# Kernel optimization log

Hardware: AMD Instinct MI355X
Metric: run time of the kernel (lower is better)

Reference implementation:

```python
import jax, jax.numpy as jnp
import numpy as np

B, T, C = 1, 4096, 2048
NH, HS, NQG = 16, 128, 4          # n_head, head_size, n_query_groups (GQA)
Q_PER_KV = NH // NQG              # 4
QKV_DIM = (NH + 2 * NQG) * HS     # 3072
ROT = HS // 2                     # rotary half-dim = 64


def setup_inputs() -> dict:
    key = jax.random.key(0)
    k0, k1, k2 = jax.random.split(key, 3)
    x = jax.random.normal(k0, (B, T, C), dtype=jnp.float32)
    W_attn = jax.random.normal(k1, (QKV_DIM, C), dtype=jnp.float32) * 0.02
    W_proj = jax.random.normal(k2, (C, C), dtype=jnp.float32) * 0.02
    # RoPE cache: cos/sin of shape (T, head_size/2), flash-attn convention
    inv_freq = 1.0 / (10000.0 ** (jnp.arange(0, HS, 2, dtype=jnp.float32) / HS))
    freqs = jnp.arange(T, dtype=jnp.float32)[:, None] * inv_freq[None, :]
    return {"x": x, "cos": jnp.cos(freqs), "sin": jnp.sin(freqs),
            "W_attn": W_attn, "W_proj": W_proj}


def _apply_rope(t, cos, sin):
    # t: (B, T, H, HS); cos/sin: (T, ROT). Non-interleaved (rotate-half) form.
    x1, x2 = t[..., :ROT], t[..., ROT:]
    c = cos[None, :, None, :]
    s = sin[None, :, None, :]
    return jnp.concatenate([x1 * c - x2 * s, x2 * c + x1 * s], axis=-1)


def reference(x, cos, sin, W_attn, W_proj):
    Bx, Tx, Cx = x.shape
    qkv = jnp.einsum('btc,fc->btf', x, W_attn)                 # (B,T,3072)
    qkv = qkv.reshape(Bx, Tx, NQG, Q_PER_KV + 2, HS)
    q = qkv[:, :, :, :Q_PER_KV, :].reshape(Bx, Tx, NH, HS)     # (B,T,16,128)
    k = qkv[:, :, :, Q_PER_KV, :]                              # (B,T,4,128)
    v = qkv[:, :, :, Q_PER_KV + 1, :]                          # (B,T,4,128)
    q = _apply_rope(q, cos, sin)
    k = _apply_rope(k, cos, sin)
    # GQA: expand kv groups to match query heads (repeat_interleave on head dim)
    k = jnp.repeat(k, Q_PER_KV, axis=2)                        # (B,T,16,128)
    v = jnp.repeat(v, Q_PER_KV, axis=2)
    scale = 1.0 / np.sqrt(HS).astype(np.float32)
    scores = jnp.einsum('bthd,bshd->bhts', q, k) * scale       # (B,H,T,T)
    causal = jnp.tril(jnp.ones((Tx, Tx), dtype=bool))
    scores = jnp.where(causal[None, None], scores, jnp.finfo(scores.dtype).min)
    attn = jax.nn.softmax(scores, axis=-1)
    y = jnp.einsum('bhts,bshd->bthd', attn, v).reshape(Bx, Tx, Cx)
    return jnp.einsum('btc,oc->bto', y, W_proj)
```

## Files before the change

kernel.cpp:

```cpp
#include <hip/hip_runtime.h>
#include <hip/hip_bf16.h>

typedef __hip_bfloat16 bf16;
typedef __attribute__((ext_vector_type(8))) short short8;
typedef __attribute__((ext_vector_type(4))) short short4v;
typedef __attribute__((ext_vector_type(4))) float floatx4;

#define T_SEQ 4096
#define C_DIM 2048
#define NHEAD 16
#define HSZ   128
#define NGRP  4

#define MFMA_BF16(A,B,C) __builtin_amdgcn_mfma_f32_16x16x32_bf16((A),(B),(C),0,0,0)

__device__ __forceinline__ void gld_lds16(const bf16* g, bf16* l) {
  __builtin_amdgcn_global_load_lds(
      (__attribute__((address_space(1))) void*)(g),
      (__attribute__((address_space(3))) void*)(l), 16, 0, 0);
}

__global__ void cvt_kernel(const float* __restrict__ src, bf16* __restrict__ dst, long n)
{
  const long i = ((long)blockIdx.x * blockDim.x + threadIdx.x) * 8;
  if (i >= n) return;
  const float4 a = *(const float4*)(src + i);
  const float4 b = *(const float4*)(src + i + 4);
  bf16 tmp[8];
  tmp[0] = __float2bfloat16(a.x); tmp[1] = __float2bfloat16(a.y);
  tmp[2] = __float2bfloat16(a.z); tmp[3] = __float2bfloat16(a.w);
  tmp[4] = __float2bfloat16(b.x); tmp[5] = __float2bfloat16(b.y);
  tmp[6] = __float2bfloat16(b.z); tmp[7] = __float2bfloat16(b.w);
  *(short8*)(dst + i) = *(const short8*)tmp;
}

__global__ __launch_bounds__(256, 3)
void gemm_bt_kernel(const bf16* __restrict__ A, const bf16* __restrict__ B,
                    float* __restrict__ Cf, bf16* __restrict__ Cq,
                    bf16* __restrict__ Ck, bf16* __restrict__ Cvt,
                    int K, int qkv_mode)
{
  __shared__ alignas(16) bf16 As[128 * 64];
  __shared__ alignas(16) bf16 Bs[128 * 64];

  const int t  = threadIdx.x;
  const int w  = t >> 6, l = t & 63;
  const int wr = w >> 1, wc = w & 1;
  const int q4 = l >> 4, ln = l & 15;
  const long bm = (long)blockIdx.y * 128;
  const long bn = (long)blockIdx.x * 128;

  floatx4 acc[4][4] = {};

  const bf16* Ab = A + (bm + t / 8) * (long)K + (t % 8) * 8;
  const bf16* Bb = B + (bn + t / 8) * (long)K + (t % 8) * 8;

  for (int k0 = 0; k0 < K; k0 += 64) {
    __syncthreads();
#pragma unroll
    for (int i = 0; i < 4; ++i) {
      gld_lds16(Ab + (long)i * 32 * K + k0, As + (i * 256 + w * 64) * 8);
      gld_lds16(Bb + (long)i * 32 * K + k0, Bs + (i * 256 + w * 64) * 8);
    }
    __syncthreads();
#pragma unroll
    for (int kk = 0; kk < 64; kk += 32) {
      short8 af[4], bfr[4];
      const int co = kk + q4 * 8;
#pragma unroll
      for (int mi = 0; mi < 4; ++mi)
        af[mi] = *(const short8*)(As + (wr * 64 + mi * 16 + ln) * 64 + co);
#pragma unroll
      for (int ni = 0; ni < 4; ++ni)
        bfr[ni] = *(const short8*)(Bs + (wc * 64 + ni * 16 + ln) * 64 + co);
#pragma unroll
      for (int mi = 0; mi < 4; ++mi)
#pragma unroll
        for (int ni = 0; ni < 4; ++ni)
          acc[mi][ni] = MFMA_BF16(af[mi], bfr[ni], acc[mi][ni]);
    }
  }

  if (!qkv_mode) {
#pragma unroll
    for (int mi = 0; mi < 4; ++mi) {
      const long r0 = bm + wr * 64 + mi * 16 + q4 * 4;
#pragma unroll
      for (int ni = 0; ni < 4; ++ni) {
        const long c = bn + wc * 64 + ni * 16 + ln;
#pragma unroll
        for (int r = 0; r < 4; ++r)
          Cf[(r0 + r) * C_DIM + c] = acc[mi][ni][r];
      }
    }
  } else {
    const int cb = blockIdx.x;
    const int g = cb / 6, slot = cb - g * 6;
    if (slot == 5) {
      bf16* dstv = Cvt + (long)g * HSZ * T_SEQ;
#pragma unroll
      for (int pass = 0; pass < 2; ++pass) {
        __syncthreads();
        if (wc == pass) {
#pragma unroll
          for (int mi = 0; mi < 4; ++mi) {
            const int tc = wr * 64 + mi * 16 + q4 * 4;
#pragma unroll
            for (int ni = 0; ni < 4; ++ni) {
              const int dr = ni * 16 + ln;
              short4v pk;
#pragma unroll
              for (int r = 0; r < 4; ++r) {
                bf16 v = __float2bfloat16(acc[mi][ni][r]);
                pk[r] = *(short*)&v;
              }
              *(short4v*)(As + dr * 128 + tc) = pk;
            }
          }
        }
        __syncthreads();
        const int row = t >> 2, ch = (t & 3) * 32;
        bf16* gp = dstv + (long)(pass * 64 + row) * T_SEQ + bm + ch;
#pragma unroll
        for (int jj = 0; jj < 4; ++jj)
          *(short8*)(gp + jj * 8) = *(const short8*)(As + row * 128 + ch + jj * 8);
      }
    } else {
      bf16* dst = (slot < 4) ? (Cq + (long)(g * 4 + slot) * T_SEQ * HSZ)
                             : (Ck + (long)g * T_SEQ * HSZ);
#pragma unroll
      for (int mi = 0; mi < 4; ++mi) {
        const long r0 = bm + wr * 64 + mi * 16 + q4 * 4;
#pragma unroll
        for (int ni = 0; ni < 4; ++ni) {
          const long c = wc * 64 + ni * 16 + ln;
#pragma unroll
          for (int r = 0; r < 4; ++r)
            dst[(r0 + r) * HSZ + c] = __float2bfloat16(acc[mi][ni][r]);
        }
      }
    }
  }
}

__global__ void rope_kernel(bf16* __restrict__ Q, bf16* __restrict__ Kb,
                            const float* __restrict__ cs, const float* __restrict__ sn)
{
  const long idx = (long)blockIdx.x * blockDim.x + threadIdx.x;
  const long NQ = (long)NHEAD * T_SEQ * 8;
  bf16* buf; long rem; float qs;
  if (idx < NQ) { buf = Q;  rem = idx;      qs = 0.08838834764831845f * 1.4426950408889634f; }
  else          { buf = Kb; rem = idx - NQ; qs = 1.0f; }
  const int d0 = (int)(rem & 7) * 8;
  const int tt = (int)((rem >> 3) & (T_SEQ - 1));
  const int hh = (int)(rem >> 15);
  const float4 c0 = *(const float4*)(cs + tt * 64 + d0);
  const float4 c1 = *(const float4*)(cs + tt * 64 + d0 + 4);
  const float4 s0 = *(const float4*)(sn + tt * 64 + d0);
  const float4 s1 = *(const float4*)(sn + tt * 64 + d0 + 4);
  float cc[8] = {c0.x,c0.y,c0.z,c0.w,c1.x,c1.y,c1.z,c1.w};
  float ss[8] = {s0.x,s0.y,s0.z,s0.w,s1.x,s1.y,s1.z,s1.w};
  bf16* p = buf + ((long)hh * T_SEQ + tt) * HSZ + d0;
  short8 v1 = *(const short8*)(p);
  short8 v2 = *(const short8*)(p + 64);
  short8 o1, o2;
#pragma unroll
  for (int jj = 0; jj < 8; ++jj) {
    short u1 = v1[jj], u2 = v2[jj];
    const float x1 = __bfloat162float(*(bf16*)&u1);
    const float x2 = __bfloat162float(*(bf16*)&u2);
    bf16 y1 = __float2bfloat16((x1 * cc[jj] - x2 * ss[jj]) * qs);
    bf16 y2 = __float2bfloat16((x2 * cc[jj] + x1 * ss[jj]) * qs);
    o1[jj] = *(short*)&y1; o2[jj] = *(short*)&y2;
  }
  *(short8*)(p)      = o1;
  *(short8*)(p + 64) = o2;
}

__global__ __launch_bounds__(256, 2)
void attn_kernel(const bf16* __restrict__ Qg, const bf16* __restrict__ Kg,
                 const bf16* __restrict__ Vtg, bf16* __restrict__ Y,
                 bf16* __restrict__ Opart, float* __restrict__ Lpart)
{
  __shared__ alignas(16) bf16 Ks[64][132];
  __shared__ alignas(16) bf16 Vt[128][68];
  __shared__ alignas(16) bf16 Ps[128][68];

  const int id  = blockIdx.x;
  const int h   = id >> 5;
  const int r   = id & 31;
  const int c   = r >> 1;
  const int isA = r & 1;
  const int g   = h >> 2;

  const int t = threadIdx.x;
  const int w = t >> 6, l = t & 63;
  const int q4 = l >> 4, ln = l & 15;

  const bf16* Qh = Qg + (long)h * T_SEQ * HSZ;
  const bf16* Kh = Kg + (long)g * T_SEQ * HSZ;
  const bf16* Vh = Vtg + (long)g * HSZ * T_SEQ;

  short8 ones_f;
#pragma unroll
  for (int i = 0; i < 8; ++i) ones_f[i] = (ln == 0) ? (short)0x3F80 : (short)0;

  const int krow = t >> 4, kc = (t & 15) * 8;
  const int vrow = t >> 3, vc = (t & 7) * 8;

  const int nph = isA ? 2 : 1;
  for (int ph = 0; ph < nph; ++ph) {
    const int P      = (isA && ph == 0) ? c : (31 - c);
    const int jlo    = (isA && ph == 1) ? 33 : 0;
    const int jhi    = isA ? (ph == 0 ? (2 * c + 2) : (64 - 2 * c)) : 33;
    const bool direct = (isA && ph == 0);
    const int qbase  = P * 128 + w * 32;

    short8 qf[2][4];
#pragma unroll
    for (int mi = 0; mi < 2; ++mi) {
      const long row = qbase + mi * 16 + ln;
#pragma unroll
      for (int ks = 0; ks < 4; ++ks)
        qf[mi][ks] = *(const short8*)(Qh + row * HSZ + ks * 32 + q4 * 8);
    }

    floatx4 acc[2][8] = {};
    floatx4 acc_l[2] = {};

    short8 kpre[4], vpre[4];
    {
      const int sb = jlo * 64;
#pragma unroll
      for (int i = 0; i < 4; ++i) {
        kpre[i] = *(const short8*)(Kh + (long)(sb + krow + 16 * i) * HSZ + kc);
        vpre[i] = *(const short8*)(Vh + (long)(vrow + 32 * i) * T_SEQ + sb + vc);
      }
    }

    for (int j = jlo; j < jhi; ++j) {
      const int s0 = j * 64;
#pragma unroll
      for (int i = 0; i < 4; ++i) {
        *(short8*)(&Ks[krow + 16 * i][kc]) = kpre[i];
        *(short8*)(&Vt[vrow + 32 * i][vc]) = vpre[i];
      }
      __syncthreads();
      if (j + 1 < jhi) {
        const int s1 = s0 + 64;
#pragma unroll
        for (int i = 0; i < 4; ++i) {
          kpre[i] = *(const short8*)(Kh + (long)(s1 + krow + 16 * i) * HSZ + kc);
          vpre[i] = *(const short8*)(Vh + (long)(vrow + 32 * i) * T_SEQ + s1 + vc);
        }
      }

      floatx4 sacc[2][4] = {};
#pragma unroll
      for (int ks = 0; ks < 4; ++ks) {
        short8 kf[4];
#pragma unroll
        for (int ni = 0; ni < 4; ++ni)
          kf[ni] = *(const short8*)(&Ks[ni * 16 + ln][ks * 32 + q4 * 8]);
#pragma unroll
        for (int mi = 0; mi < 2; ++mi)
#pragma unroll
          for (int ni = 0; ni < 4; ++ni)
            sacc[mi][ni] = MFMA_BF16(qf[mi][ks], kf[ni], sacc[mi][ni]);
      }

#pragma unroll
      for (int mi = 0; mi < 2; ++mi) {
        const int base_m = qbase + mi * 16 + q4 * 4 - s0 - ln;
#pragma unroll
        for (int ni = 0; ni < 4; ++ni)
#pragma unroll
          for (int r2 = 0; r2 < 4; ++r2) {
            float pv = __builtin_amdgcn_exp2f(sacc[mi][ni][r2]);
            if (base_m + r2 - ni * 16 < 0) pv = 0.f;
            Ps[w * 32 + mi * 16 + q4 * 4 + r2][ni * 16 + ln] = __float2bfloat16(pv);
          }
      }

#pragma unroll
      for (int ks = 0; ks < 2; ++ks) {
        short8 pf[2], vf[8];
#pragma unroll
        for (int mi = 0; mi < 2; ++mi)
          pf[mi] = *(const short8*)(&Ps[w * 32 + mi * 16 + ln][ks * 32 + q4 * 8]);
#pragma unroll
        for (int nd = 0; nd < 8; ++nd)
          vf[nd] = *(const short8*)(&Vt[nd * 16 + ln][ks * 32 + q4 * 8]);
#pragma unroll
        for (int mi = 0; mi < 2; ++mi) {
          acc_l[mi] = MFMA_BF16(pf[mi], ones_f, acc_l[mi]);
#pragma unroll
          for (int nd = 0; nd < 8; ++nd)
            acc[mi][nd] = MFMA_BF16(pf[mi], vf[nd], acc[mi][nd]);
        }
      }
      __syncthreads();
    }

    if (direct) {
#pragma unroll
      for (int mi = 0; mi < 2; ++mi) {
#pragma unroll
        for (int r2 = 0; r2 < 4; ++r2) {
          const float lv = __shfl(acc_l[mi][r2], l & 48, 64);
          const float inv = (lv > 0.f) ? 1.f / lv : 0.f;
          const long tq = qbase + mi * 16 + q4 * 4 + r2;
#pragma unroll
          for (int nd = 0; nd < 8; ++nd)
            Y[tq * C_DIM + h * HSZ + nd * 16 + ln] = __float2bfloat16(acc[mi][nd][r2] * inv);
        }
      }
    } else {
      const int sidx = (h * 16 + (15 - c)) * 2 + isA;
      bf16* Op = Opart + (long)sidx * (128 * 128);
      float* Lp = Lpart + sidx * 128;
#pragma unroll
      for (int mi = 0; mi < 2; ++mi) {
#pragma unroll
        for (int r2 = 0; r2 < 4; ++r2) {
          const int row = w * 32 + mi * 16 + q4 * 4 + r2;
          if (ln == 0) Lp[row] = acc_l[mi][r2];
#pragma unroll
          for (int nd = 0; nd < 8; ++nd)
            Op[row * 128 + nd * 16 + ln] = __float2bfloat16(acc[mi][nd][r2]);
        }
      }
    }
  }
}

__global__ void combine_kernel(const bf16* __restrict__ Opart,
                               const float* __restrict__ Lpart,
                               bf16* __restrict__ Y)
{
  const int b = blockIdx.x;
  const int h = b >> 4, pp = b & 15;
  const bf16* O0 = Opart + (long)b * 2 * 16384;
  const bf16* O1 = O0 + 16384;
  const float* L0 = Lpart + b * 256;
  const float* L1 = L0 + 128;
  const long qb = (long)(pp + 16) * 128;
  const int t = threadIdx.x;
#pragma unroll
  for (int it = 0; it < 8; ++it) {
    const int idx = it * 2048 + t * 8;
    const int row = idx >> 7, d = idx & 127;
    const float lsum = L0[row] + L1[row];
    const float inv = (lsum > 0.f) ? 1.f / lsum : 0.f;
    const short8 a = *(const short8*)(O0 + idx);
    const short8 bb = *(const short8*)(O1 + idx);
    short8 o;
#pragma unroll
    for (int jj = 0; jj < 8; ++jj) {
      short ua = a[jj], ub = bb[jj];
      const float fa = __bfloat162float(*(bf16*)&ua);
      const float fb = __bfloat162float(*(bf16*)&ub);
      bf16 y = __float2bfloat16((fa + fb) * inv);
      o[jj] = *(short*)&y;
    }
    *(short8*)(Y + (qb + row) * C_DIM + h * HSZ + d) = o;
  }
}

extern "C" void kernel_launch(void* const* d_in, const int* in_sizes, int n_in,
                              void* d_out, int out_size, void* d_ws, size_t ws_size,
                              hipStream_t stream)
{
  const float* x  = (const float*)d_in[0];
  const float* cs = (const float*)d_in[1];
  const float* sn = (const float*)d_in[2];
  const float* Wa = (const float*)d_in[3];
  const float* Wp = (const float*)d_in[4];
  float* out = (float*)d_out;

  const long nx  = (long)T_SEQ * C_DIM;
  const long nwa = (long)(NHEAD + 2 * NGRP) * HSZ * C_DIM;
  const long nwp = (long)C_DIM * C_DIM;
  const long nqh = (long)NHEAD * T_SEQ * HSZ;
  const long nkg = (long)NGRP * T_SEQ * HSZ;

  const size_t need = (size_t)(nx + nwa + nqh + 2 * nkg + nqh) * sizeof(bf16);
  if (ws_size < need) return;

  bf16* xb  = (bf16*)d_ws;
  bf16* Wab = xb + nx;
  bf16* Q   = Wab + nwa;
  bf16* K   = Q + nqh;
  bf16* Vt  = K + nkg;
  bf16* Y   = Vt + nkg;
  bf16* Wpb = Q;
  bf16* Opart = xb;
  float* Lpart = (float*)Wab;

  cvt_kernel<<<(int)(nx  / 8 / 256), 256, 0, stream>>>(x,  xb,  nx);
  cvt_kernel<<<(int)(nwa / 8 / 256), 256, 0, stream>>>(Wa, Wab, nwa);
  gemm_bt_kernel<<<dim3(24, 32), 256, 0, stream>>>(xb, Wab, nullptr, Q, K, Vt, C_DIM, 1);
  rope_kernel<<<2560, 256, 0, stream>>>(Q, K, cs, sn);
  attn_kernel<<<512, 256, 0, stream>>>(Q, K, Vt, Y, Opart, Lpart);
  combine_kernel<<<256, 256, 0, stream>>>(Opart, Lpart, Y);
  cvt_kernel<<<(int)(nwp / 8 / 256), 256, 0, stream>>>(Wp, Wpb, nwp);
  gemm_bt_kernel<<<dim3(16, 32), 256, 0, stream>>>(Y, Wpb, out, nullptr, nullptr, nullptr, C_DIM, 0);
}
```

Measured before the change: 335.6 us.

## Split causal attention work into three balanced slices per query-block pair

Replaces the two-way split of each causal query-block pair with a three-way split of KV ranges, so 768 attention blocks each get about 22 KV tiles. The combine kernel is generalized to sum 2 or 3 partial outputs per query block. Launch bounds are raised to 3 blocks per CU to fit the larger grid in one wave on the 256-CU device. The aim is better load balance and occupancy, at the cost of more partial-output traffic and register pressure.

```diff
diff --git a/kernel.cpp b/kernel.cpp
--- a/kernel.cpp
+++ b/kernel.cpp
@@ -177,7 +177,7 @@
   *(short8*)(p + 64) = o2;
 }
 
-__global__ __launch_bounds__(256, 2)
+__global__ __launch_bounds__(256, 3)
 void attn_kernel(const bf16* __restrict__ Qg, const bf16* __restrict__ Kg,
                  const bf16* __restrict__ Vtg, bf16* __restrict__ Y,
                  bf16* __restrict__ Opart, float* __restrict__ Lpart)
@@ -187,11 +187,34 @@
   __shared__ alignas(16) bf16 Ps[128][68];
 
   const int id  = blockIdx.x;
-  const int h   = id >> 5;
-  const int r   = id & 31;
-  const int c   = r >> 1;
-  const int isA = r & 1;
+  const int h   = id / 48;
+  const int r   = id - h * 48;
+  const int c   = r / 3;
+  const int sl  = r - c * 3;
   const int g   = h >> 2;
+
+  int segP[2], segLo[2], segHi[2], segPs[2], nseg;
+  bool segDir[2] = {false, false};
+  if (c <= 10) {
+    if (sl == 0) { nseg = 2;
+      segP[0] = c;      segLo[0] = 0;  segHi[0] = 2 * c + 2; segPs[0] = 0; segDir[0] = true;
+      segP[1] = 31 - c; segLo[1] = 44; segHi[1] = 64 - 2 * c; segPs[1] = 0;
+    } else if (sl == 1) { nseg = 1;
+      segP[0] = 31 - c; segLo[0] = 0;  segHi[0] = 22; segPs[0] = 1;
+    } else { nseg = 1;
+      segP[0] = 31 - c; segLo[0] = 22; segHi[0] = 44; segPs[0] = 2;
+    }
+  } else {
+    if (sl == 0) { nseg = 1;
+      segP[0] = c;      segLo[0] = 0;  segHi[0] = 22; segPs[0] = 0;
+    } else if (sl == 1) { nseg = 2;
+      segP[0] = c;      segLo[0] = 22; segHi[0] = 2 * c + 2;  segPs[0] = 1;
+      segP[1] = 31 - c; segLo[1] = 0;  segHi[1] = 42 - 2 * c; segPs[1] = 2;
+    } else { nseg = 1;
+      segP[0] = 31 - c; segLo[0] = 42 - 2 * c; segHi[0] = 64 - 2 * c; segPs[0] = 3;
+    }
+  }
+  const int pairBase = h * 53 + ((c <= 10) ? c * 3 : 33 + (c - 11) * 4);
 
   const int t = threadIdx.x;
   const int w = t >> 6, l = t & 63;
@@ -208,13 +231,11 @@
   const int krow = t >> 4, kc = (t & 15) * 8;
   const int vrow = t >> 3, vc = (t & 7) * 8;
 
-  const int nph = isA ? 2 : 1;
-  for (int ph = 0; ph < nph; ++ph) {
-    const int P      = (isA && ph == 0) ? c : (31 - c);
-    const int jlo    = (isA && ph == 1) ? 33 : 0;
-    const int jhi    = isA ? (ph == 0 ? (2 * c + 2) : (64 - 2 * c)) : 33;
-    const bool direct = (isA && ph == 0);
-    const int qbase  = P * 128 + w * 32;
+  for (int ph = 0; ph < nseg; ++ph) {
+    const int P   = segP[ph];
+    const int jlo = segLo[ph], jhi = segHi[ph];
+    const bool direct = segDir[ph];
+    const int qbase = P * 128 + w * 32;
 
     short8 qf[2][4];
 #pragma unroll
@@ -316,7 +337,7 @@
         }
       }
     } else {
-      const int sidx = (h * 16 + (15 - c)) * 2 + isA;
+      const int sidx = pairBase + segPs[ph];
       bf16* Op = Opart + (long)sidx * (128 * 128);
       float* Lp = Lpart + sidx * 128;
 #pragma unroll
@@ -338,29 +359,40 @@
                                const float* __restrict__ Lpart,
                                bf16* __restrict__ Y)
 {
-  const int b = blockIdx.x;
-  const int h = b >> 4, pp = b & 15;
-  const bf16* O0 = Opart + (long)b * 2 * 16384;
-  const bf16* O1 = O0 + 16384;
-  const float* L0 = Lpart + b * 256;
-  const float* L1 = L0 + 128;
-  const long qb = (long)(pp + 16) * 128;
+  const int cid = blockIdx.x;
+  const int h = cid / 21, u = cid - h * 21;
+  int P, sbase, ns;
+  if (u < 11) {
+    const int c = u; P = 31 - c; sbase = h * 53 + c * 3; ns = 3;
+  } else {
+    const int v = u - 11;
+    const int c = 11 + (v >> 1);
+    const int pb = h * 53 + 33 + (c - 11) * 4;
+    if (!(v & 1)) { P = c;      sbase = pb;     ns = 2; }
+    else          { P = 31 - c; sbase = pb + 2; ns = 2; }
+  }
+  const long qb = (long)P * 128;
   const int t = threadIdx.x;
 #pragma unroll
   for (int it = 0; it < 8; ++it) {
     const int idx = it * 2048 + t * 8;
     const int row = idx >> 7, d = idx & 127;
-    const float lsum = L0[row] + L1[row];
+    float lsum = 0.f;
+    float osum[8] = {0.f, 0.f, 0.f, 0.f, 0.f, 0.f, 0.f, 0.f};
+    for (int k = 0; k < ns; ++k) {
+      lsum += Lpart[(sbase + k) * 128 + row];
+      const short8 a = *(const short8*)(Opart + (long)(sbase + k) * 16384 + idx);
+#pragma unroll
+      for (int jj = 0; jj < 8; ++jj) {
+        short ua = a[jj];
+        osum[jj] += __bfloat162float(*(bf16*)&ua);
+      }
+    }
     const float inv = (lsum > 0.f) ? 1.f / lsum : 0.f;
-    const short8 a = *(const short8*)(O0 + idx);
-    const short8 bb = *(const short8*)(O1 + idx);
     short8 o;
 #pragma unroll
     for (int jj = 0; jj < 8; ++jj) {
-      short ua = a[jj], ub = bb[jj];
-      const float fa = __bfloat162float(*(bf16*)&ua);
-      const float fb = __bfloat162float(*(bf16*)&ub);
-      bf16 y = __float2bfloat16((fa + fb) * inv);
+      bf16 y = __float2bfloat16(osum[jj] * inv);
       o[jj] = *(short*)&y;
     }
     *(short8*)(Y + (qb + row) * C_DIM + h * HSZ + d) = o;
@@ -395,14 +427,14 @@
   bf16* Y   = Vt + nkg;
   bf16* Wpb = Q;
   bf16* Opart = xb;
-  float* Lpart = (float*)Wab;
+  float* Lpart = (float*)(xb + 848L * 16384);
 
   cvt_kernel<<<(int)(nx  / 8 / 256), 256, 0, stream>>>(x,  xb,  nx);
   cvt_kernel<<<(int)(nwa / 8 / 256), 256, 0, stream>>>(Wa, Wab, nwa);
   gemm_bt_kernel<<<dim3(24, 32), 256, 0, stream>>>(xb, Wab, nullptr, Q, K, Vt, C_DIM, 1);
   rope_kernel<<<2560, 256, 0, stream>>>(Q, K, cs, sn);
-  attn_kernel<<<512, 256, 0, stream>>>(Q, K, Vt, Y, Opart, Lpart);
-  combine_kernel<<<256, 256, 0, stream>>>(Opart, Lpart, Y);
+  attn_kernel<<<768, 256, 0, stream>>>(Q, K, Vt, Y, Opart, Lpart);
+  combine_kernel<<<336, 256, 0, stream>>>(Opart, Lpart, Y);
   cvt_kernel<<<(int)(nwp / 8 / 256), 256, 0, stream>>>(Wp, Wpb, nwp);
   gemm_bt_kernel<<<dim3(16, 32), 256, 0, stream>>>(Y, Wpb, out, nullptr, nullptr, nullptr, C_DIM, 0);
 }
```

Result: slower. 463.2 us (+38.0%).

## Fuse RoPE and Q scaling into the QKV GEMM epilogue

Applied to the files above, without the earlier changes.

Removes the standalone RoPE kernel and applies the rotary embedding and query scaling inside the QKV GEMM epilogue. The accumulator tile is staged through padded shared memory so each thread holds both rotary halves of a row, then written with vectorized stores. This saves one kernel launch and a full read-modify-write pass over Q and K in global memory. In exchange, shared memory per block grows from 32 KB to about 33 KB, which could affect occupancy under the 3-blocks launch bound, and the epilogue adds loads of the cos/sin tables.

```diff
diff --git a/kernel.cpp b/kernel.cpp
--- a/kernel.cpp
+++ b/kernel.cpp
@@ -38,10 +38,12 @@
 void gemm_bt_kernel(const bf16* __restrict__ A, const bf16* __restrict__ B,
                     float* __restrict__ Cf, bf16* __restrict__ Cq,
                     bf16* __restrict__ Ck, bf16* __restrict__ Cvt,
+                    const float* __restrict__ cs, const float* __restrict__ sn,
                     int K, int qkv_mode)
 {
-  __shared__ alignas(16) bf16 As[128 * 64];
-  __shared__ alignas(16) bf16 Bs[128 * 64];
+  __shared__ alignas(16) bf16 smem[128 * 132];
+  bf16* As = smem;
+  bf16* Bs = smem + 128 * 64;
 
   const int t  = threadIdx.x;
   const int w  = t >> 6, l = t & 63;
@@ -128,53 +130,50 @@
     } else {
       bf16* dst = (slot < 4) ? (Cq + (long)(g * 4 + slot) * T_SEQ * HSZ)
                              : (Ck + (long)g * T_SEQ * HSZ);
+      const float qs = (slot < 4) ? (0.08838834764831845f * 1.4426950408889634f) : 1.0f;
+      __syncthreads();
+      bf16* Ts = smem;
 #pragma unroll
       for (int mi = 0; mi < 4; ++mi) {
-        const long r0 = bm + wr * 64 + mi * 16 + q4 * 4;
+        const int tl0 = wr * 64 + mi * 16 + q4 * 4;
 #pragma unroll
         for (int ni = 0; ni < 4; ++ni) {
-          const long c = wc * 64 + ni * 16 + ln;
+          const int cc = wc * 64 + ni * 16 + ln;
 #pragma unroll
           for (int r = 0; r < 4; ++r)
-            dst[(r0 + r) * HSZ + c] = __float2bfloat16(acc[mi][ni][r]);
-        }
+            Ts[(tl0 + r) * 132 + cc] = __float2bfloat16(acc[mi][ni][r]);
+        }
+      }
+      __syncthreads();
+      const int tl = t >> 1, d0 = (t & 1) * 32;
+      const long trow = bm + tl;
+      bf16* gp = dst + trow * HSZ;
+#pragma unroll
+      for (int dj = 0; dj < 4; ++dj) {
+        const int d = d0 + dj * 8;
+        const short8 v1 = *(const short8*)(Ts + tl * 132 + d);
+        const short8 v2 = *(const short8*)(Ts + tl * 132 + d + 64);
+        const float4 c0 = *(const float4*)(cs + trow * 64 + d);
+        const float4 c1 = *(const float4*)(cs + trow * 64 + d + 4);
+        const float4 s0 = *(const float4*)(sn + trow * 64 + d);
+        const float4 s1 = *(const float4*)(sn + trow * 64 + d + 4);
+        const float ccv[8] = {c0.x,c0.y,c0.z,c0.w,c1.x,c1.y,c1.z,c1.w};
+        const float ssv[8] = {s0.x,s0.y,s0.z,s0.w,s1.x,s1.y,s1.z,s1.w};
+        short8 o1, o2;
+#pragma unroll
+        for (int jj = 0; jj < 8; ++jj) {
+          short u1 = v1[jj], u2 = v2[jj];
+          const float x1 = __bfloat162float(*(bf16*)&u1);
+          const float x2 = __bfloat162float(*(bf16*)&u2);
+          bf16 y1 = __float2bfloat16((x1 * ccv[jj] - x2 * ssv[jj]) * qs);
+          bf16 y2 = __float2bfloat16((x2 * ccv[jj] + x1 * ssv[jj]) * qs);
+          o1[jj] = *(short*)&y1; o2[jj] = *(short*)&y2;
+        }
+        *(short8*)(gp + d) = o1;
+        *(short8*)(gp + d + 64) = o2;
       }
     }
   }
-}
-
-__global__ void rope_kernel(bf16* __restrict__ Q, bf16* __restrict__ Kb,
-                            const float* __restrict__ cs, const float* __restrict__ sn)
-{
-  const long idx = (long)blockIdx.x * blockDim.x + threadIdx.x;
-  const long NQ = (long)NHEAD * T_SEQ * 8;
-  bf16* buf; long rem; float qs;
-  if (idx < NQ) { buf = Q;  rem = idx;      qs = 0.08838834764831845f * 1.4426950408889634f; }
-  else          { buf = Kb; rem = idx - NQ; qs = 1.0f; }
-  const int d0 = (int)(rem & 7) * 8;
-  const int tt = (int)((rem >> 3) & (T_SEQ - 1));
-  const int hh = (int)(rem >> 15);
-  const float4 c0 = *(const float4*)(cs + tt * 64 + d0);
-  const float4 c1 = *(const float4*)(cs + tt * 64 + d0 + 4);
-  const float4 s0 = *(const float4*)(sn + tt * 64 + d0);
-  const float4 s1 = *(const float4*)(sn + tt * 64 + d0 + 4);
-  float cc[8] = {c0.x,c0.y,c0.z,c0.w,c1.x,c1.y,c1.z,c1.w};
-  float ss[8] = {s0.x,s0.y,s0.z,s0.w,s1.x,s1.y,s1.z,s1.w};
-  bf16* p = buf + ((long)hh * T_SEQ + tt) * HSZ + d0;
-  short8 v1 = *(const short8*)(p);
-  short8 v2 = *(const short8*)(p + 64);
-  short8 o1, o2;
-#pragma unroll
-  for (int jj = 0; jj < 8; ++jj) {
-    short u1 = v1[jj], u2 = v2[jj];
-    const float x1 = __bfloat162float(*(bf16*)&u1);
-    const float x2 = __bfloat162float(*(bf16*)&u2);
-    bf16 y1 = __float2bfloat16((x1 * cc[jj] - x2 * ss[jj]) * qs);
-    bf16 y2 = __float2bfloat16((x2 * cc[jj] + x1 * ss[jj]) * qs);
-    o1[jj] = *(short*)&y1; o2[jj] = *(short*)&y2;
-  }
-  *(short8*)(p)      = o1;
-  *(short8*)(p + 64) = o2;
 }
 
 __global__ __launch_bounds__(256, 2)
@@ -399,10 +398,9 @@
 
   cvt_kernel<<<(int)(nx  / 8 / 256), 256, 0, stream>>>(x,  xb,  nx);
   cvt_kernel<<<(int)(nwa / 8 / 256), 256, 0, stream>>>(Wa, Wab, nwa);
-  gemm_bt_kernel<<<dim3(24, 32), 256, 0, stream>>>(xb, Wab, nullptr, Q, K, Vt, C_DIM, 1);
-  rope_kernel<<<2560, 256, 0, stream>>>(Q, K, cs, sn);
+  gemm_bt_kernel<<<dim3(24, 32), 256, 0, stream>>>(xb, Wab, nullptr, Q, K, Vt, cs, sn, C_DIM, 1);
   attn_kernel<<<512, 256, 0, stream>>>(Q, K, Vt, Y, Opart, Lpart);
   combine_kernel<<<256, 256, 0, stream>>>(Opart, Lpart, Y);
   cvt_kernel<<<(int)(nwp / 8 / 256), 256, 0, stream>>>(Wp, Wpb, nwp);
-  gemm_bt_kernel<<<dim3(16, 32), 256, 0, stream>>>(Y, Wpb, out, nullptr, nullptr, nullptr, C_DIM, 0);
-}
+  gemm_bt_kernel<<<dim3(16, 32), 256, 0, stream>>>(Y, Wpb, out, nullptr, nullptr, nullptr, nullptr, nullptr, C_DIM, 0);
+}
```

Measured after the change: 335.2 us. Within noise of the previous version (-0.1%).
